# Optimization experiments

Hardware: AMD Instinct MI355X
Metric: run time of the kernel (lower is better)

The kernel has to match this reference:

```python
import jax, jax.numpy as jnp
import numpy as np

N_DATA = 500000
EMB = 256
K = 4096
BS = 64
T = 0.07
M = 0.5


def _l2norm(x, axis=-1, eps=1e-12):
    return x / jnp.maximum(jnp.linalg.norm(x, axis=axis, keepdims=True), eps)


def setup_inputs() -> dict:
    key = jax.random.key(0)
    k1, k2, k3, k4, k5, k6 = jax.random.split(key, 6)
    vis_feat = jax.random.normal(k1, (BS, EMB), dtype=jnp.float32)
    text_feat = jax.random.normal(k2, (BS, EMB), dtype=jnp.float32)
    # memory banks: original inits uniform in [-stdv, stdv]; randn scaled works the same numerically
    stdv = 1.0 / np.sqrt(EMB / 3)
    vis_memory = jax.random.uniform(k3, (N_DATA, EMB), dtype=jnp.float32, minval=-stdv, maxval=stdv)
    text_memory = jax.random.uniform(k4, (N_DATA, EMB), dtype=jnp.float32, minval=-stdv, maxval=stdv)
    idx = jax.random.randint(k5, (BS,), 0, N_DATA, dtype=jnp.int32)
    slct_idx = jax.random.randint(k6, (BS, K + 1), 0, N_DATA, dtype=jnp.int32)
    # column 0 holds the positive index, as in slct_idx.select(1,0).copy_(idx)
    slct_idx = slct_idx.at[:, 0].set(idx)
    return {
        "vis_feat": vis_feat,
        "text_feat": text_feat,
        "vis_memory": vis_memory,
        "text_memory": text_memory,
        "slct_idx": slct_idx,
        "idx": idx,
    }


def reference(vis_feat, text_feat, vis_memory, text_memory, slct_idx, idx):
    # embeddings are L2-normalized before use (nn.functional.normalize(dim=1))
    vn = _l2norm(vis_feat)   # [bs, D]
    tn = _l2norm(text_feat)  # [bs, D]

    # gather K+1 negatives/positive from memory banks (detached in original)
    tf = jax.lax.stop_gradient(text_memory[slct_idx])  # [bs, K+1, D]
    vf = jax.lax.stop_gradient(vis_memory[slct_idx])   # [bs, K+1, D]

    # batched dot products + exp(./T) (bmm with [bs, D, 1])
    vis_out = jnp.exp(jnp.einsum("bkd,bd->bk", tf, vn) / T)   # [bs, K+1]
    text_out = jnp.exp(jnp.einsum("bkd,bd->bk", vf, tn) / T)  # [bs, K+1]

    # NCE normalization constants, set on first pass: Z = mean * N_data
    Z_v = jax.lax.stop_gradient(jnp.mean(vis_out)) * N_DATA
    Z_t = jax.lax.stop_gradient(jnp.mean(text_out)) * N_DATA
    vis_out = vis_out / Z_v
    text_out = text_out / Z_t

    # EMA memory update + renormalize + scatter (no_grad in original)
    vis_pos = vis_memory[idx] * M + jax.lax.stop_gradient(vn) * (1.0 - M)
    text_pos = text_memory[idx] * M + jax.lax.stop_gradient(tn) * (1.0 - M)
    new_vis_memory = vis_memory.at[idx].set(_l2norm(vis_pos))
    new_text_memory = text_memory.at[idx].set(_l2norm(text_pos))

    return vis_out, text_out, new_vis_memory, new_text_memory
```

## Files before the change

kernel.cpp:

```cpp
#include <hip/hip_runtime.h>

#define NDATA 500000
#define EMB   256
#define BS    64
#define KP1   4097
#define NPAIR (BS * KP1)
#define INV_T (1.0f / 0.07f)

#define SCAN_EPB 2048
#define NB_SCAN  ((NDATA + SCAN_EPB - 1) / SCAN_EPB)
#define RPW      32
#define NWAVES   (NDATA / RPW)
#define NBLKF    ((NWAVES + 3) / 4)
#define SCALE_BLKS ((2 * NPAIR + 255) / 256)
#define NBY      17

typedef float    f32x4 __attribute__((ext_vector_type(4)));
typedef unsigned u32x4 __attribute__((ext_vector_type(4)));

__global__ __launch_bounds__(256) void norm_hist_kernel(
    const float* __restrict__ vis_feat, const float* __restrict__ text_feat,
    float* __restrict__ vn, float* __restrict__ tn,
    const int* __restrict__ slct, unsigned* __restrict__ counts,
    unsigned* __restrict__ old) {
  int bid = blockIdx.x;
  if (bid < 128) {
    int b = bid & 63;
    bool is_vis = bid < 64;
    const float* src = (is_vis ? vis_feat : text_feat) + b * EMB;
    float* dst = (is_vis ? vn : tn) + b * EMB;
    int t = threadIdx.x;
    float x = src[t];
    float s = x * x;
    for (int off = 32; off > 0; off >>= 1) s += __shfl_down(s, off, 64);
    __shared__ float red[4];
    if ((t & 63) == 0) red[t >> 6] = s;
    __syncthreads();
    float norm = sqrtf(red[0] + red[1] + red[2] + red[3]);
    dst[t] = x / fmaxf(norm, 1e-12f);
  } else {
    int i = (bid - 128) * 256 + threadIdx.x;
    if (i < NPAIR) {
      int r = slct[i];
      old[i] = atomicAdd(&counts[r], 1u);
    }
  }
}

__global__ __launch_bounds__(256) void scan1_kernel(
    const unsigned* __restrict__ counts, unsigned* __restrict__ start,
    unsigned* __restrict__ bsum) {
  int t = threadIdx.x;
  int base = blockIdx.x * SCAN_EPB + t * 8;
  unsigned v[8];
  unsigned tsum = 0;
#pragma unroll
  for (int j = 0; j < 8; ++j) {
    int i = base + j;
    unsigned c = (i < NDATA) ? counts[i] : 0u;
    v[j] = tsum;
    tsum += c;
  }
  unsigned x = tsum;
  for (int d = 1; d < 64; d <<= 1) {
    unsigned y = __shfl_up(x, d, 64);
    if ((t & 63) >= d) x += y;
  }
  __shared__ unsigned wsum[4];
  if ((t & 63) == 63) wsum[t >> 6] = x;
  __syncthreads();
  unsigned woff = 0;
  for (int wv = 0; wv < (t >> 6); ++wv) woff += wsum[wv];
  unsigned ex = woff + x - tsum;
#pragma unroll
  for (int j = 0; j < 8; ++j) {
    int i = base + j;
    if (i < NDATA) start[i] = ex + v[j];
  }
  if (t == 255) bsum[blockIdx.x] = woff + x;
}

__global__ __launch_bounds__(256) void scan2_kernel(unsigned* __restrict__ bsum) {
  int t = threadIdx.x;
  unsigned v = (t < NB_SCAN) ? bsum[t] : 0u;
  unsigned x = v;
  for (int d = 1; d < 64; d <<= 1) {
    unsigned y = __shfl_up(x, d, 64);
    if ((t & 63) >= d) x += y;
  }
  __shared__ unsigned wsum[4];
  if ((t & 63) == 63) wsum[t >> 6] = x;
  __syncthreads();
  unsigned woff = 0;
  for (int wv = 0; wv < (t >> 6); ++wv) woff += wsum[wv];
  unsigned ex = woff + x - v;
  if (t < NB_SCAN) bsum[t] = ex;
}

__global__ __launch_bounds__(256) void scatter_kernel(
    const int* __restrict__ slct, const unsigned* __restrict__ start,
    const unsigned* __restrict__ bsum, const unsigned* __restrict__ old,
    unsigned* __restrict__ pairs) {
  int i = blockIdx.x * 256 + threadIdx.x;
  if (i < NPAIR) {
    int r = slct[i];
    unsigned pos = start[r] + bsum[r >> 11] + old[i];
    int b = i / KP1;
    int kk = i - b * KP1;
    pairs[pos] = ((unsigned)b << 13) | (unsigned)kk;
  }
}

#define LOADC(R, rb)                                                          \
  { _Pragma("unroll") for (int j = 0; j < 8; ++j)                             \
      R[j] = __builtin_nontemporal_load(&s4[(size_t)((rb) + j) * 64 + lane]); }

#define STOREC(R, rb)                                                         \
  { _Pragma("unroll") for (int j = 0; j < 8; ++j)                             \
      __builtin_nontemporal_store(R[j], &d4[(size_t)((rb) + j) * 64 + lane]); }

#define REFS(R, rb)                                                           \
  { u32x4 c0 = *(const u32x4*)&counts[(rb)];                                  \
    u32x4 c1 = *(const u32x4*)&counts[(rb) + 4];                              \
    u32x4 s0 = *(const u32x4*)&start[(rb)];                                   \
    u32x4 s1 = *(const u32x4*)&start[(rb) + 4];                               \
    unsigned cn[8] = {c0.x, c0.y, c0.z, c0.w, c1.x, c1.y, c1.z, c1.w};        \
    unsigned sn[8] = {s0.x, s0.y, s0.z, s0.w, s1.x, s1.y, s1.z, s1.w};        \
    _Pragma("unroll") for (int j = 0; j < 8; ++j) {                           \
      unsigned n = cn[j];                                                     \
      if (n) {                                                                \
        unsigned gs = sn[j] + bs;                                             \
        unsigned p = pairs[gs];                                               \
        f32x4 fv = f4[(p >> 13) * 64 + lane];                                 \
        for (unsigned u = 0; u < n; ++u) {                                    \
          unsigned pn = p; f32x4 fvn = fv;                                    \
          if (u + 1 < n) {                                                    \
            pn = pairs[gs + u + 1];                                           \
            fvn = f4[(pn >> 13) * 64 + lane];                                 \
          }                                                                   \
          float d = R[j].x * fv.x + R[j].y * fv.y + R[j].z * fv.z + R[j].w * fv.w; \
          for (int off = 32; off > 0; off >>= 1) d += __shfl_down(d, off, 64);\
          if (lane == 0) {                                                    \
            float e = __expf(d * INV_T);                                      \
            outz[(p >> 13) * KP1 + (p & 8191u)] = e;                          \
            local += e;                                                       \
          }                                                                   \
          p = pn; fv = fvn;                                                   \
        }                                                                     \
      }                                                                       \
    } }

__global__ __launch_bounds__(256) void fused_copy_dot_kernel(
    const float* __restrict__ text_mem, const float* __restrict__ vis_mem,
    float* __restrict__ out_text, float* __restrict__ out_vis,
    const float* __restrict__ vn, const float* __restrict__ tn,
    const unsigned* __restrict__ counts, const unsigned* __restrict__ start,
    const unsigned* __restrict__ bsum, const unsigned* __restrict__ pairs,
    float* __restrict__ out, float* __restrict__ zsum) {
  int z = blockIdx.z;
  const f32x4* s4 = (const f32x4*)(z == 0 ? text_mem : vis_mem);
  f32x4* d4 = (f32x4*)(z == 0 ? out_text : out_vis);
  const f32x4* f4 = (const f32x4*)(z == 0 ? vn : tn);
  float* outz = out + (size_t)z * NPAIR;

  int t = threadIdx.x, w = t >> 6, lane = t & 63;
  int gw = blockIdx.x * 4 + w;
  float local = 0.f;

  if (gw < NWAVES) {
    int r0 = gw * RPW;
    unsigned bs = bsum[r0 >> 11];
    f32x4 A[8], B[8];
    LOADC(A, r0);
    LOADC(B, r0 + 8);
    STOREC(A, r0);      REFS(A, r0);
    LOADC(A, r0 + 16);
    STOREC(B, r0 + 8);  REFS(B, r0 + 8);
    LOADC(B, r0 + 24);
    STOREC(A, r0 + 16); REFS(A, r0 + 16);
    STOREC(B, r0 + 24); REFS(B, r0 + 24);
  }
  __shared__ float red[4];
  if (lane == 0) red[w] = local;
  __syncthreads();
  if (t == 0) {
    float s = red[0] + red[1] + red[2] + red[3];
    atomicAdd(&zsum[z], s);
  }
}

__global__ __launch_bounds__(256) void scale_update_kernel(
    float* __restrict__ out, const float* __restrict__ zsum,
    const float* __restrict__ vis_mem, const float* __restrict__ text_mem,
    const float* __restrict__ vn, const float* __restrict__ tn,
    const int* __restrict__ idx,
    float* __restrict__ out_vis, float* __restrict__ out_text) {
  int bid = blockIdx.x;
  if (bid < SCALE_BLKS) {
    int i = bid * 256 + threadIdx.x;
    if (i < 2 * NPAIR) {
      float Z = ((i < NPAIR) ? zsum[0] : zsum[1]) * ((float)NDATA / (float)NPAIR);
      out[i] = out[i] / Z;
    }
  } else {
    int bb = bid - SCALE_BLKS;
    int b = bb & 63;
    bool is_vis = bb < 64;
    int row = idx[b];
    for (int b2 = b + 1; b2 < BS; ++b2)
      if (idx[b2] == row) return;
    const float* mem  = (is_vis ? vis_mem : text_mem) + (size_t)row * EMB;
    const float* feat = (is_vis ? vn : tn) + b * EMB;
    float* dst = (is_vis ? out_vis : out_text) + (size_t)row * EMB;
    int t = threadIdx.x;
    float p = mem[t] * 0.5f + feat[t] * 0.5f;
    float s = p * p;
    for (int off = 32; off > 0; off >>= 1) s += __shfl_down(s, off, 64);
    __shared__ float red[4];
    if ((t & 63) == 0) red[t >> 6] = s;
    __syncthreads();
    float norm = sqrtf(red[0] + red[1] + red[2] + red[3]);
    dst[t] = p / fmaxf(norm, 1e-12f);
  }
}

__global__ __launch_bounds__(256) void dot_exp_kernel(
    const float* __restrict__ text_mem, const float* __restrict__ vis_mem,
    const float* __restrict__ vn, const float* __restrict__ tn,
    const int* __restrict__ slct, float* __restrict__ out,
    float* __restrict__ partials) {
  int b = blockIdx.x;
  int z = blockIdx.z;
  const float* mem  = (z == 0) ? text_mem : vis_mem;
  const float* feat = (z == 0) ? vn : tn;
  float* o = out + (size_t)z * NPAIR + (size_t)b * KP1;
  const int* srow = slct + b * KP1;
  __shared__ float4 sf[64];
  int t = threadIdx.x;
  if (t < 64) sf[t] = ((const float4*)(feat + b * EMB))[t];
  __syncthreads();
  int w = t >> 6, lane = t & 63;
  float4 f = sf[lane];
  int kbase = blockIdx.y * 256 + w * 64;
  int kend  = min(kbase + 64, KP1);
  float local = 0.f;
  int k = kbase;
  for (; k + 2 <= kend; k += 2) {
    int r0 = srow[k], r1 = srow[k + 1];
    float4 v0 = ((const float4*)(mem + (size_t)r0 * EMB))[lane];
    float4 v1 = ((const float4*)(mem + (size_t)r1 * EMB))[lane];
    float p0 = v0.x * f.x + v0.y * f.y + v0.z * f.z + v0.w * f.w;
    float p1 = v1.x * f.x + v1.y * f.y + v1.z * f.z + v1.w * f.w;
    for (int off = 32; off > 0; off >>= 1) {
      p0 += __shfl_down(p0, off, 64);
      p1 += __shfl_down(p1, off, 64);
    }
    if (lane == 0) {
      float e0 = __expf(p0 * INV_T);
      float e1 = __expf(p1 * INV_T);
      o[k] = e0; o[k + 1] = e1;
      local += e0 + e1;
    }
  }
  if (k < kend) {
    int r0 = srow[k];
    float4 v0 = ((const float4*)(mem + (size_t)r0 * EMB))[lane];
    float p0 = v0.x * f.x + v0.y * f.y + v0.z * f.z + v0.w * f.w;
    for (int off = 32; off > 0; off >>= 1) p0 += __shfl_down(p0, off, 64);
    if (lane == 0) { float e0 = __expf(p0 * INV_T); o[k] = e0; local += e0; }
  }
  __shared__ float red[4];
  if (lane == 0) red[w] = local;
  __syncthreads();
  if (t == 0)
    partials[((size_t)z * NBY + blockIdx.y) * BS + b] =
        red[0] + red[1] + red[2] + red[3];
}

__global__ __launch_bounds__(256) void reduce_z_kernel(
    const float* __restrict__ partials, float* __restrict__ zsum, int per_z) {
  int z = blockIdx.x;
  const float* p = partials + (size_t)z * per_z;
  float s = 0.f;
  for (int i = threadIdx.x; i < per_z; i += 256) s += p[i];
  for (int off = 32; off > 0; off >>= 1) s += __shfl_down(s, off, 64);
  __shared__ float red[4];
  if ((threadIdx.x & 63) == 0) red[threadIdx.x >> 6] = s;
  __syncthreads();
  if (threadIdx.x == 0) zsum[z] = red[0] + red[1] + red[2] + red[3];
}

__global__ __launch_bounds__(256) void copy2_kernel(
    const float4* __restrict__ src_a, float4* __restrict__ dst_a,
    const float4* __restrict__ src_b, float4* __restrict__ dst_b, long n4) {
  long i = (long)blockIdx.x * blockDim.x + threadIdx.x;
  long stride = (long)gridDim.x * blockDim.x;
  for (; i < 2 * n4; i += stride) {
    if (i < n4) dst_a[i] = src_a[i];
    else        dst_b[i - n4] = src_b[i - n4];
  }
}

extern "C" void kernel_launch(void* const* d_in, const int* in_sizes, int n_in,
                              void* d_out, int out_size, void* d_ws, size_t ws_size,
                              hipStream_t stream) {
  const float* vis_feat  = (const float*)d_in[0];
  const float* text_feat = (const float*)d_in[1];
  const float* vis_mem   = (const float*)d_in[2];
  const float* text_mem  = (const float*)d_in[3];
  const int*   slct      = (const int*)d_in[4];
  const int*   idx       = (const int*)d_in[5];

  float* out          = (float*)d_out;
  float* out_vis_mem  = out + (size_t)2 * NPAIR;
  float* out_text_mem = out_vis_mem + (size_t)NDATA * EMB;

  float*    ws     = (float*)d_ws;
  float*    zsum   = ws;
  unsigned* counts = (unsigned*)(zsum + 4);
  unsigned* start  = counts + NDATA;
  unsigned* bsum   = start + NDATA;
  unsigned* old    = bsum + 256;
  unsigned* pairs  = old + NPAIR;
  float*    vn     = (float*)(pairs + NPAIR);
  float*    tn     = vn + BS * EMB;
  size_t needed = ((size_t)(4 + 2 * NDATA + 256 + 2 * NPAIR) +
                   (size_t)(2 * BS * EMB)) * 4;

  if (ws_size >= needed) {
    hipMemsetAsync(zsum, 0, (4 + NDATA) * sizeof(unsigned), stream);
    norm_hist_kernel<<<128 + (NPAIR + 255) / 256, 256, 0, stream>>>(
        vis_feat, text_feat, vn, tn, slct, counts, old);
    scan1_kernel<<<NB_SCAN, 256, 0, stream>>>(counts, start, bsum);
    scan2_kernel<<<1, 256, 0, stream>>>(bsum);
    scatter_kernel<<<(NPAIR + 255) / 256, 256, 0, stream>>>(slct, start, bsum, old, pairs);

    dim3 gF(NBLKF, 1, 2);
    fused_copy_dot_kernel<<<gF, 256, 0, stream>>>(
        text_mem, vis_mem, out_text_mem, out_vis_mem, vn, tn,
        counts, start, bsum, pairs, out, zsum);
  } else {
    norm_hist_kernel<<<128, 256, 0, stream>>>(
        vis_feat, text_feat, vn, tn, slct, counts, old);
    dim3 gB(BS, NBY, 2);
    dot_exp_kernel<<<gB, 256, 0, stream>>>(text_mem, vis_mem, vn, tn, slct, out,
                                           (float*)old);
    reduce_z_kernel<<<2, 256, 0, stream>>>((float*)old, zsum, NBY * BS);
    const long n4 = (long)NDATA * EMB / 4;
    copy2_kernel<<<8192, 256, 0, stream>>>(
        (const float4*)vis_mem,  (float4*)out_vis_mem,
        (const float4*)text_mem, (float4*)out_text_mem, n4);
  }

  scale_update_kernel<<<SCALE_BLKS + 128, 256, 0, stream>>>(
      out, zsum, vis_mem, text_mem, vn, tn, idx, out_vis_mem, out_text_mem);
}
```

Before: 432.5 us.

## Write dot results in sorted order and scatter them during scaling

```diff
diff --git a/kernel.cpp b/kernel.cpp
--- a/kernel.cpp
+++ b/kernel.cpp
@@ -12,6 +12,7 @@
 #define RPW      32
 #define NWAVES   (NDATA / RPW)
 #define NBLKF    ((NWAVES + 3) / 4)
+#define SSC_BLKS ((NPAIR + 255) / 256)
 #define SCALE_BLKS ((2 * NPAIR + 255) / 256)
 #define NBY      17
 
@@ -119,6 +120,8 @@
   { _Pragma("unroll") for (int j = 0; j < 8; ++j)                             \
       __builtin_nontemporal_store(R[j], &d4[(size_t)((rb) + j) * 64 + lane]); }
 
+#define DOT4(Rj, fv) (Rj.x * fv.x + Rj.y * fv.y + Rj.z * fv.z + Rj.w * fv.w)
+
 #define REFS(R, rb)                                                           \
   { u32x4 c0 = *(const u32x4*)&counts[(rb)];                                  \
     u32x4 c1 = *(const u32x4*)&counts[(rb) + 4];                              \
@@ -130,22 +133,40 @@
       unsigned n = cn[j];                                                     \
       if (n) {                                                                \
         unsigned gs = sn[j] + bs;                                             \
-        unsigned p = pairs[gs];                                               \
-        f32x4 fv = f4[(p >> 13) * 64 + lane];                                 \
-        for (unsigned u = 0; u < n; ++u) {                                    \
-          unsigned pn = p; f32x4 fvn = fv;                                    \
-          if (u + 1 < n) {                                                    \
-            pn = pairs[gs + u + 1];                                           \
-            fvn = f4[(pn >> 13) * 64 + lane];                                 \
+        unsigned u = 0;                                                       \
+        for (; u + 4 <= n; u += 4) {                                          \
+          unsigned p0 = pairs[gs + u],     p1 = pairs[gs + u + 1];            \
+          unsigned p2 = pairs[gs + u + 2], p3 = pairs[gs + u + 3];            \
+          f32x4 f0 = f4[(p0 >> 13) * 64 + lane];                              \
+          f32x4 f1 = f4[(p1 >> 13) * 64 + lane];                              \
+          f32x4 f2 = f4[(p2 >> 13) * 64 + lane];                              \
+          f32x4 f3 = f4[(p3 >> 13) * 64 + lane];                              \
+          float d0 = DOT4(R[j], f0), d1 = DOT4(R[j], f1);                     \
+          float d2 = DOT4(R[j], f2), d3 = DOT4(R[j], f3);                     \
+          for (int off = 32; off > 0; off >>= 1) {                            \
+            d0 += __shfl_down(d0, off, 64);                                   \
+            d1 += __shfl_down(d1, off, 64);                                   \
+            d2 += __shfl_down(d2, off, 64);                                   \
+            d3 += __shfl_down(d3, off, 64);                                   \
           }                                                                   \
-          float d = R[j].x * fv.x + R[j].y * fv.y + R[j].z * fv.z + R[j].w * fv.w; \
+          if (lane == 0) {                                                    \
+            float e0 = __expf(d0 * INV_T), e1 = __expf(d1 * INV_T);           \
+            float e2 = __expf(d2 * INV_T), e3 = __expf(d3 * INV_T);           \
+            tz[gs + u] = e0; tz[gs + u + 1] = e1;                             \
+            tz[gs + u + 2] = e2; tz[gs + u + 3] = e3;                         \
+            local += (e0 + e1) + (e2 + e3);                                   \
+          }                                                                   \
+        }                                                                     \
+        for (; u < n; ++u) {                                                  \
+          unsigned p = pairs[gs + u];                                         \
+          f32x4 fv = f4[(p >> 13) * 64 + lane];                               \
+          float d = DOT4(R[j], fv);                                           \
           for (int off = 32; off > 0; off >>= 1) d += __shfl_down(d, off, 64);\
           if (lane == 0) {                                                    \
             float e = __expf(d * INV_T);                                      \
-            outz[(p >> 13) * KP1 + (p & 8191u)] = e;                          \
+            tz[gs + u] = e;                                                   \
             local += e;                                                       \
           }                                                                   \
-          p = pn; fv = fvn;                                                   \
         }                                                                     \
       }                                                                       \
     } }
@@ -156,12 +177,13 @@
     const float* __restrict__ vn, const float* __restrict__ tn,
     const unsigned* __restrict__ counts, const unsigned* __restrict__ start,
     const unsigned* __restrict__ bsum, const unsigned* __restrict__ pairs,
-    float* __restrict__ out, float* __restrict__ zsum) {
+    float* __restrict__ tmp0, float* __restrict__ tmp1,
+    float* __restrict__ zsum) {
   int z = blockIdx.z;
   const f32x4* s4 = (const f32x4*)(z == 0 ? text_mem : vis_mem);
   f32x4* d4 = (f32x4*)(z == 0 ? out_text : out_vis);
   const f32x4* f4 = (const f32x4*)(z == 0 ? vn : tn);
-  float* outz = out + (size_t)z * NPAIR;
+  float* tz = (z == 0) ? tmp0 : tmp1;
 
   int t = threadIdx.x, w = t >> 6, lane = t & 63;
   int gw = blockIdx.x * 4 + w;
@@ -186,6 +208,123 @@
   if (t == 0) {
     float s = red[0] + red[1] + red[2] + red[3];
     atomicAdd(&zsum[z], s);
+  }
+}
+
+__global__ __launch_bounds__(256) void scatter_scale_update_kernel(
+    const unsigned* __restrict__ pairs,
+    const float* __restrict__ tmp0, const float* __restrict__ tmp1,
+    float* __restrict__ out, const float* __restrict__ zsum,
+    const float* __restrict__ vis_mem, const float* __restrict__ text_mem,
+    const float* __restrict__ vn, const float* __restrict__ tn,
+    const int* __restrict__ idx,
+    float* __restrict__ out_vis, float* __restrict__ out_text) {
+  int bid = blockIdx.x;
+  if (bid < SSC_BLKS) {
+    int pos = bid * 256 + threadIdx.x;
+    if (pos < NPAIR) {
+      const float c = (float)NDATA / (float)NPAIR;
+      unsigned p = pairs[pos];
+      int o = (int)(p >> 13) * KP1 + (int)(p & 8191u);
+      out[o]         = tmp0[pos] / (zsum[0] * c);
+      out[NPAIR + o] = tmp1[pos] / (zsum[1] * c);
+    }
+  } else {
+    int bb = bid - SSC_BLKS;
+    int b = bb & 63;
+    bool is_vis = bb < 64;
+    int row = idx[b];
+    for (int b2 = b + 1; b2 < BS; ++b2)
+      if (idx[b2] == row) return;
+    const float* mem  = (is_vis ? vis_mem : text_mem) + (size_t)row * EMB;
+    const float* feat = (is_vis ? vn : tn) + b * EMB;
+    float* dst = (is_vis ? out_vis : out_text) + (size_t)row * EMB;
+    int t = threadIdx.x;
+    float p = mem[t] * 0.5f + feat[t] * 0.5f;
+    float s = p * p;
+    for (int off = 32; off > 0; off >>= 1) s += __shfl_down(s, off, 64);
+    __shared__ float red[4];
+    if ((t & 63) == 0) red[t >> 6] = s;
+    __syncthreads();
+    float norm = sqrtf(red[0] + red[1] + red[2] + red[3]);
+    dst[t] = p / fmaxf(norm, 1e-12f);
+  }
+}
+
+__global__ __launch_bounds__(256) void dot_exp_kernel(
+    const float* __restrict__ text_mem, const float* __restrict__ vis_mem,
+    const float* __restrict__ vn, const float* __restrict__ tn,
+    const int* __restrict__ slct, float* __restrict__ out,
+    float* __restrict__ partials) {
+  int b = blockIdx.x;
+  int z = blockIdx.z;
+  const float* mem  = (z == 0) ? text_mem : vis_mem;
+  const float* feat = (z == 0) ? vn : tn;
+  float* o = out + (size_t)z * NPAIR + (size_t)b * KP1;
+  const int* srow = slct + b * KP1;
+  __shared__ float4 sf[64];
+  int t = threadIdx.x;
+  if (t < 64) sf[t] = ((const float4*)(feat + b * EMB))[t];
+  __syncthreads();
+  int w = t >> 6, lane = t & 63;
+  float4 f = sf[lane];
+  int kbase = blockIdx.y * 256 + w * 64;
+  int kend  = min(kbase + 64, KP1);
+  float local = 0.f;
+  int k = kbase;
+  for (; k + 2 <= kend; k += 2) {
+    int r0 = srow[k], r1 = srow[k + 1];
+    float4 v0 = ((const float4*)(mem + (size_t)r0 * EMB))[lane];
+    float4 v1 = ((const float4*)(mem + (size_t)r1 * EMB))[lane];
+    float p0 = v0.x * f.x + v0.y * f.y + v0.z * f.z + v0.w * f.w;
+    float p1 = v1.x * f.x + v1.y * f.y + v1.z * f.z + v1.w * f.w;
+    for (int off = 32; off > 0; off >>= 1) {
+      p0 += __shfl_down(p0, off, 64);
+      p1 += __shfl_down(p1, off, 64);
+    }
+    if (lane == 0) {
+      float e0 = __expf(p0 * INV_T);
+      float e1 = __expf(p1 * INV_T);
+      o[k] = e0; o[k + 1] = e1;
+      local += e0 + e1;
+    }
+  }
+  if (k < kend) {
+    int r0 = srow[k];
+    float4 v0 = ((const float4*)(mem + (size_t)r0 * EMB))[lane];
+    float p0 = v0.x * f.x + v0.y * f.y + v0.z * f.z + v0.w * f.w;
+    for (int off = 32; off > 0; off >>= 1) p0 += __shfl_down(p0, off, 64);
+    if (lane == 0) { float e0 = __expf(p0 * INV_T); o[k] = e0; local += e0; }
+  }
+  __shared__ float red[4];
+  if (lane == 0) red[w] = local;
+  __syncthreads();
+  if (t == 0)
+    partials[((size_t)z * NBY + blockIdx.y) * BS + b] =
+        red[0] + red[1] + red[2] + red[3];
+}
+
+__global__ __launch_bounds__(256) void reduce_z_kernel(
+    const float* __restrict__ partials, float* __restrict__ zsum, int per_z) {
+  int z = blockIdx.x;
+  const float* p = partials + (size_t)z * per_z;
+  float s = 0.f;
+  for (int i = threadIdx.x; i < per_z; i += 256) s += p[i];
+  for (int off = 32; off > 0; off >>= 1) s += __shfl_down(s, off, 64);
+  __shared__ float red[4];
+  if ((threadIdx.x & 63) == 0) red[threadIdx.x >> 6] = s;
+  __syncthreads();
+  if (threadIdx.x == 0) zsum[z] = red[0] + red[1] + red[2] + red[3];
+}
+
+__global__ __launch_bounds__(256) void copy2_kernel(
+    const float4* __restrict__ src_a, float4* __restrict__ dst_a,
+    const float4* __restrict__ src_b, float4* __restrict__ dst_b, long n4) {
+  long i = (long)blockIdx.x * blockDim.x + threadIdx.x;
+  long stride = (long)gridDim.x * blockDim.x;
+  for (; i < 2 * n4; i += stride) {
+    if (i < n4) dst_a[i] = src_a[i];
+    else        dst_b[i - n4] = src_b[i - n4];
   }
 }
 
@@ -224,83 +363,6 @@
   }
 }
 
-__global__ __launch_bounds__(256) void dot_exp_kernel(
-    const float* __restrict__ text_mem, const float* __restrict__ vis_mem,
-    const float* __restrict__ vn, const float* __restrict__ tn,
-    const int* __restrict__ slct, float* __restrict__ out,
-    float* __restrict__ partials) {
-  int b = blockIdx.x;
-  int z = blockIdx.z;
-  const float* mem  = (z == 0) ? text_mem : vis_mem;
-  const float* feat = (z == 0) ? vn : tn;
-  float* o = out + (size_t)z * NPAIR + (size_t)b * KP1;
-  const int* srow = slct + b * KP1;
-  __shared__ float4 sf[64];
-  int t = threadIdx.x;
-  if (t < 64) sf[t] = ((const float4*)(feat + b * EMB))[t];
-  __syncthreads();
-  int w = t >> 6, lane = t & 63;
-  float4 f = sf[lane];
-  int kbase = blockIdx.y * 256 + w * 64;
-  int kend  = min(kbase + 64, KP1);
-  float local = 0.f;
-  int k = kbase;
-  for (; k + 2 <= kend; k += 2) {
-    int r0 = srow[k], r1 = srow[k + 1];
-    float4 v0 = ((const float4*)(mem + (size_t)r0 * EMB))[lane];
-    float4 v1 = ((const float4*)(mem + (size_t)r1 * EMB))[lane];
-    float p0 = v0.x * f.x + v0.y * f.y + v0.z * f.z + v0.w * f.w;
-    float p1 = v1.x * f.x + v1.y * f.y + v1.z * f.z + v1.w * f.w;
-    for (int off = 32; off > 0; off >>= 1) {
-      p0 += __shfl_down(p0, off, 64);
-      p1 += __shfl_down(p1, off, 64);
-    }
-    if (lane == 0) {
-      float e0 = __expf(p0 * INV_T);
-      float e1 = __expf(p1 * INV_T);
-      o[k] = e0; o[k + 1] = e1;
-      local += e0 + e1;
-    }
-  }
-  if (k < kend) {
-    int r0 = srow[k];
-    float4 v0 = ((const float4*)(mem + (size_t)r0 * EMB))[lane];
-    float p0 = v0.x * f.x + v0.y * f.y + v0.z * f.z + v0.w * f.w;
-    for (int off = 32; off > 0; off >>= 1) p0 += __shfl_down(p0, off, 64);
-    if (lane == 0) { float e0 = __expf(p0 * INV_T); o[k] = e0; local += e0; }
-  }
-  __shared__ float red[4];
-  if (lane == 0) red[w] = local;
-  __syncthreads();
-  if (t == 0)
-    partials[((size_t)z * NBY + blockIdx.y) * BS + b] =
-        red[0] + red[1] + red[2] + red[3];
-}
-
-__global__ __launch_bounds__(256) void reduce_z_kernel(
-    const float* __restrict__ partials, float* __restrict__ zsum, int per_z) {
-  int z = blockIdx.x;
-  const float* p = partials + (size_t)z * per_z;
-  float s = 0.f;
-  for (int i = threadIdx.x; i < per_z; i += 256) s += p[i];
-  for (int off = 32; off > 0; off >>= 1) s += __shfl_down(s, off, 64);
-  __shared__ float red[4];
-  if ((threadIdx.x & 63) == 0) red[threadIdx.x >> 6] = s;
-  __syncthreads();
-  if (threadIdx.x == 0) zsum[z] = red[0] + red[1] + red[2] + red[3];
-}
-
-__global__ __launch_bounds__(256) void copy2_kernel(
-    const float4* __restrict__ src_a, float4* __restrict__ dst_a,
-    const float4* __restrict__ src_b, float4* __restrict__ dst_b, long n4) {
-  long i = (long)blockIdx.x * blockDim.x + threadIdx.x;
-  long stride = (long)gridDim.x * blockDim.x;
-  for (; i < 2 * n4; i += stride) {
-    if (i < n4) dst_a[i] = src_a[i];
-    else        dst_b[i - n4] = src_b[i - n4];
-  }
-}
-
 extern "C" void kernel_launch(void* const* d_in, const int* in_sizes, int n_in,
                               void* d_out, int out_size, void* d_ws, size_t ws_size,
                               hipStream_t stream) {
@@ -322,9 +384,11 @@
   unsigned* bsum   = start + NDATA;
   unsigned* old    = bsum + 256;
   unsigned* pairs  = old + NPAIR;
-  float*    vn     = (float*)(pairs + NPAIR);
+  float*    tmp1   = (float*)(pairs + NPAIR);
+  float*    vn     = tmp1 + NPAIR;
   float*    tn     = vn + BS * EMB;
-  size_t needed = ((size_t)(4 + 2 * NDATA + 256 + 2 * NPAIR) +
+  float*    tmp0   = (float*)old;
+  size_t needed = ((size_t)(4 + 2 * NDATA + 256 + 3 * NPAIR) +
                    (size_t)(2 * BS * EMB)) * 4;
 
   if (ws_size >= needed) {
@@ -338,7 +402,11 @@
     dim3 gF(NBLKF, 1, 2);
     fused_copy_dot_kernel<<<gF, 256, 0, stream>>>(
         text_mem, vis_mem, out_text_mem, out_vis_mem, vn, tn,
-        counts, start, bsum, pairs, out, zsum);
+        counts, start, bsum, pairs, tmp0, tmp1, zsum);
+
+    scatter_scale_update_kernel<<<SSC_BLKS + 128, 256, 0, stream>>>(
+        pairs, tmp0, tmp1, out, zsum, vis_mem, text_mem, vn, tn, idx,
+        out_vis_mem, out_text_mem);
   } else {
     norm_hist_kernel<<<128, 256, 0, stream>>>(
         vis_feat, text_feat, vn, tn, slct, counts, old);
@@ -350,8 +418,7 @@
     copy2_kernel<<<8192, 256, 0, stream>>>(
         (const float4*)vis_mem,  (float4*)out_vis_mem,
         (const float4*)text_mem, (float4*)out_text_mem, n4);
-  }
-
-  scale_update_kernel<<<SCALE_BLKS + 128, 256, 0, stream>>>(
-      out, zsum, vis_mem, text_mem, vn, tn, idx, out_vis_mem, out_text_mem);
-}
+    scale_update_kernel<<<SCALE_BLKS + 128, 256, 0, stream>>>(
+        out, zsum, vis_mem, text_mem, vn, tn, idx, out_vis_mem, out_text_mem);
+  }
+}
```

Result: faster. 421.3 us (-2.6%).
